# Kernel tuning notes

Hardware: AMD Instinct MI355X
Metric: run time of the kernel (lower is better)

## Reference

```python
import jax, jax.numpy as jnp
import numpy as np

B, N, H = 32, 1024, 512
THR = 0.05  # peak_detection_threshold


def _l2norm(x):
    return x / jnp.linalg.norm(x, axis=-1, keepdims=True)


def setup_inputs() -> dict:
    key = jax.random.key(0)
    ks = jax.random.split(key, 6)
    def w(k, shape, fan_in):
        return jax.random.normal(k, shape, jnp.float32) / np.float32(np.sqrt(fan_in))
    return {
        "segment_rep": jax.random.normal(ks[0], (B, N, H), jnp.float32),
        "phn_mask": jnp.ones((B, N), jnp.float32),
        # SegmentSimilarityMeasure: Linear(2H->H), ReLU, Linear(H->1, no bias)
        "W1": w(ks[1], (2 * H, H), 2 * H),
        "b1": jnp.zeros((H,), jnp.float32),
        "W2": w(ks[2], (H, 1), H),
        # word_enc: Linear(H->H), ReLU, Linear(H->H)
        "We1": w(ks[3], (H, H), H),
        "be1": jnp.zeros((H,), jnp.float32),
        "We2": w(ks[4], (H, H), H),
        "be2": jnp.zeros((H,), jnp.float32),
    }


def _forward(segment_rep, phn_mask, W1, b1, W2, We1, be1, We2, be2):
    Bs, Np, Hd = segment_rep.shape
    # adjacent segment similarity: MLP on concat of l2-normalized neighbors -> (B, N-1)
    cat = jnp.concatenate([_l2norm(segment_rep[:, :-1, :]), _l2norm(segment_rep[:, 1:, :])], axis=2)
    S = (jax.nn.relu(cat @ W1 + b1) @ W2)[..., 0]

    # relative dissimilarity
    Smin = jnp.min(S, axis=1, keepdims=True)
    Smax = jnp.max(S, axis=1, keepdims=True)
    D = 1.0 - (S - Smin) / (Smax - Smin)

    # peak detector (faithful to original, incl. final overwrite of first-order cols -2:)
    z = jnp.zeros_like(D)
    fo = z
    fo = fo.at[:, 0].set(jnp.maximum(D[:, 0] - D[:, 1], 0.0))
    fo = fo.at[:, 1:-1].set(jnp.minimum(jnp.maximum(D[:, 1:-1] - D[:, :-2], 0.0),
                                        jnp.maximum(D[:, 1:-1] - D[:, 2:], 0.0)))
    fo = fo.at[:, -1].set(jnp.maximum(D[:, -1] - D[:, -2], 0.0))
    so = z
    so = so.at[:, 0:2].set(jnp.maximum(D[:, 0:2] - D[:, 2:4], 0.0))
    so = so.at[:, 2:-2].set(jnp.minimum(jnp.maximum(D[:, 2:-2] - D[:, :-4], 0.0),
                                        jnp.maximum(D[:, 2:-2] - D[:, 4:], 0.0)))
    fo = fo.at[:, -2:].set(jnp.maximum(D[:, -2:] - D[:, -4:-2], 0.0))  # replicates original code
    P = jnp.minimum(jnp.maximum(jnp.maximum(fo, so) - THR, 0.0), fo)

    # pad, mask, straight-through hard boundaries
    P = jnp.pad(P, ((0, 0), (0, 1)))
    P = jax.nn.relu(P + (phn_mask - 1.0))
    b_soft = jnp.tanh(10.0 * P)
    b_hard = jnp.tanh(100000.0 * P)
    b = b_soft + jax.lax.stop_gradient(b_hard - b_soft)
    b = jnp.cumsum(b, axis=1)  # (B, N)
    b = b + (b[:, :1] == 0).astype(b.dtype)  # per-row +1 if b[:,0]==0
    num_word_segments = b[:, -1].astype(jnp.int32) + 1  # (B,)

    # U: column j holds j+1 for j < num_word_segments[i], else -100000. Nmax = N (static bound).
    cols = jnp.arange(1, Np + 1, dtype=jnp.int32)  # (Nmax,)
    U = jnp.where(cols[None, :] <= num_word_segments[:, None],
                  cols.astype(segment_rep.dtype)[None, :], -100000.0)  # (B, Nmax)

    V = U[:, None, :] - b[:, :, None]  # (B, N, Nmax)
    Wseg = 1.0 - jnp.tanh(100000.0 * jnp.abs(V))
    Wseg = Wseg / jnp.sum(Wseg, axis=1, keepdims=True)
    Wseg = jnp.nan_to_num(Wseg)

    # pool: (B, Nmax, N) @ (B, N, H) -> (B, Nmax, H)
    word_rep = jnp.einsum('bnm,bnh->bmh', Wseg, segment_rep)
    word_masks = jnp.where(word_rep == 0, 0.0, 1.0)
    out = jax.nn.relu(word_rep @ We1 + be1) @ We2 + be2
    return out * word_masks


def reference(segment_rep, phn_mask, W1, b1, W2, We1, be1, We2, be2):
    return _forward(segment_rep, phn_mask, W1, b1, W2, We1, be1, We2, be2)
```

## Files before the change

kernel.cpp:

```cpp
#include <hip/hip_runtime.h>

#define BB 32
#define NN 1024
#define HH 512
#define NS 1023

typedef unsigned short u16;
typedef unsigned int   u32;
typedef __attribute__((ext_vector_type(8))) short bf16x8;
typedef __attribute__((ext_vector_type(4))) float f32x4;

__device__ __forceinline__ float bf2f(u16 h) {
  union { u32 u; float f; } c; c.u = ((u32)h) << 16; return c.f;
}
__device__ __forceinline__ u16 f2bf(float f) {
  union { float f; u32 u; } c; c.f = f;
  u32 u = c.u;
  return (u16)((u + 0x7fffu + ((u >> 16) & 1u)) >> 16);
}
__device__ __forceinline__ void split_bf(float x, u16& hi, u16& lo) {
  hi = f2bf(x);
  lo = f2bf(x - bf2f(hi));
}

__global__ __launch_bounds__(64) void k_prep_a(const float* __restrict__ seg,
                                               u16* __restrict__ ahi,
                                               u16* __restrict__ alo) {
  int row = blockIdx.x, lane = threadIdx.x;
  const float4* p = (const float4*)(seg + ((size_t)row << 9) + lane * 8);
  float4 a = p[0], b = p[1];
  float v[8] = {a.x, a.y, a.z, a.w, b.x, b.y, b.z, b.w};
  float s = 0.f;
#pragma unroll
  for (int i = 0; i < 8; ++i) s += v[i] * v[i];
#pragma unroll
  for (int m = 32; m; m >>= 1) s += __shfl_xor(s, m, 64);
  float nrm = sqrtf(s);
  u16 h[8], l[8];
#pragma unroll
  for (int i = 0; i < 8; ++i) split_bf(v[i] / nrm, h[i], l[i]);
  size_t off = ((size_t)row << 9) + lane * 8;
  *(uint4*)(ahi + off) = make_uint4(h[0] | (h[1] << 16), h[2] | (h[3] << 16),
                                    h[4] | (h[5] << 16), h[6] | (h[7] << 16));
  *(uint4*)(alo + off) = make_uint4(l[0] | (l[1] << 16), l[2] | (l[3] << 16),
                                    l[4] | (l[5] << 16), l[6] | (l[7] << 16));
}

__global__ __launch_bounds__(256) void k_tr(const float* __restrict__ src,
                                            u16* __restrict__ dh,
                                            u16* __restrict__ dl,
                                            int K, int N) {
  __shared__ u16 Th[64 * 66], Tl[64 * 66];
  int nb = blockIdx.x * 64, kb = blockIdx.y * 64;
  int tid = threadIdx.x;
#pragma unroll
  for (int i = 0; i < 16; ++i) {
    int e = tid + i * 256;
    int r = e >> 6, c = e & 63;
    float v = src[(size_t)(kb + r) * N + nb + c];
    u16 hi, lo; split_bf(v, hi, lo);
    Th[c * 66 + r] = hi;
    Tl[c * 66 + r] = lo;
  }
  __syncthreads();
#pragma unroll
  for (int i = 0; i < 16; ++i) {
    int e = tid + i * 256;
    int n = e >> 6, k = e & 63;
    dh[(size_t)(nb + n) * K + kb + k] = Th[n * 66 + k];
    if (dl) dl[(size_t)(nb + n) * K + kb + k] = Tl[n * 66 + k];
  }
}

__global__ __launch_bounds__(256) void k_sgemm(const u16* __restrict__ ahi,
                                               const u16* __restrict__ alo,
                                               const u16* __restrict__ w1h,
                                               const u16* __restrict__ w1l,
                                               const float* __restrict__ b1,
                                               const float* __restrict__ W2,
                                               float* __restrict__ Spart) {
  __shared__ u16 Ah[64 * 40], Al_[64 * 40];
  __shared__ u16 Wh[256 * 40], Wl[256 * 40];
  __shared__ float red[4][64];

  int tid = threadIdx.x;
  int wave = tid >> 6, lane = tid & 63, quad = lane >> 4, l15 = lane & 15;
  int b = blockIdx.z, mblk = blockIdx.y, nblk = blockIdx.x;
  int rowbase = b * NN + mblk * 64;
  int ncol0 = nblk * 256;

  f32x4 acc[4][4];
#pragma unroll
  for (int mi = 0; mi < 4; ++mi)
#pragma unroll
    for (int ni = 0; ni < 4; ++ni) acc[mi][ni] = (f32x4){0.f, 0.f, 0.f, 0.f};

  for (int ks = 0; ks < 32; ++ks) {
    int k0 = ks * 32, half = k0 >> 9, cb = k0 & 511;
    __syncthreads();
#pragma unroll
    for (int it = 0; it < 2; ++it) {
      int i = tid + it * 256;
      int m = i >> 3, plane = (i >> 2) & 1, ch = i & 3;
      int grow = rowbase + m + half; if (grow > 32767) grow = 32767;
      size_t go = ((size_t)grow << 9) + cb + ch * 8;
      if (plane) *(uint4*)&Al_[m * 40 + ch * 8] = *(const uint4*)(alo + go);
      else       *(uint4*)&Ah [m * 40 + ch * 8] = *(const uint4*)(ahi + go);
    }
#pragma unroll
    for (int it = 0; it < 8; ++it) {
      int i = tid + it * 256;
      int n = i >> 3, plane = (i >> 2) & 1, ch = i & 3;
      size_t go = (size_t)(ncol0 + n) * 1024 + k0 + ch * 8;
      if (plane) *(uint4*)&Wl[n * 40 + ch * 8] = *(const uint4*)(w1l + go);
      else       *(uint4*)&Wh[n * 40 + ch * 8] = *(const uint4*)(w1h + go);
    }
    __syncthreads();

    bf16x8 a_h[4], a_l[4];
#pragma unroll
    for (int mi = 0; mi < 4; ++mi) {
      int off = (mi * 16 + l15) * 40 + quad * 8;
      a_h[mi] = *(const bf16x8*)&Ah [off];
      a_l[mi] = *(const bf16x8*)&Al_[off];
    }
#pragma unroll
    for (int ni = 0; ni < 4; ++ni) {
      int off = (wave * 64 + ni * 16 + l15) * 40 + quad * 8;
      bf16x8 b_h = *(const bf16x8*)&Wh[off];
      bf16x8 b_l = *(const bf16x8*)&Wl[off];
#pragma unroll
      for (int mi = 0; mi < 4; ++mi) {
        acc[mi][ni] = __builtin_amdgcn_mfma_f32_16x16x32_bf16(a_h[mi], b_h, acc[mi][ni], 0, 0, 0);
        acc[mi][ni] = __builtin_amdgcn_mfma_f32_16x16x32_bf16(a_h[mi], b_l, acc[mi][ni], 0, 0, 0);
        acc[mi][ni] = __builtin_amdgcn_mfma_f32_16x16x32_bf16(a_l[mi], b_h, acc[mi][ni], 0, 0, 0);
      }
    }
  }

#pragma unroll
  for (int mi = 0; mi < 4; ++mi) {
#pragma unroll
    for (int reg = 0; reg < 4; ++reg) {
      float part = 0.f;
#pragma unroll
      for (int ni = 0; ni < 4; ++ni) {
        int n_g = ncol0 + wave * 64 + ni * 16 + l15;
        float h = acc[mi][ni][reg] + b1[n_g];
        h = h > 0.f ? h : 0.f;
        part = fmaf(h, W2[n_g], part);
      }
#pragma unroll
      for (int m = 8; m; m >>= 1) part += __shfl_xor(part, m, 64);
      if (l15 == 0) red[wave][mi * 16 + quad * 4 + reg] = part;
    }
  }
  __syncthreads();
  if (tid < 64) {
    float s = red[0][tid] + red[1][tid] + red[2][tid] + red[3][tid];
    int srow = mblk * 64 + tid;
    if (srow < NS)
      Spart[((size_t)nblk * BB + b) * NN + srow] = s;
  }
}

__global__ __launch_bounds__(256) void k_row(const float* __restrict__ S0,
                                             const float* __restrict__ S1,
                                             const float* __restrict__ mask,
                                             int* __restrict__ assign,
                                             float* __restrict__ weight,
                                             float* __restrict__ total,
                                             int* __restrict__ startn,
                                             int* __restrict__ endn) {
  int b = blockIdx.x, tid = threadIdx.x;
  __shared__ float Ssh[NS];
  __shared__ float Dsh[NS];
  __shared__ float tsh[NN];
  __shared__ float bsh[NN];
  __shared__ float totl[NN];
  __shared__ int   stl[NN];
  __shared__ int   enl[NN];
  __shared__ float red[256];

  for (int n = tid; n < NS; n += 256)
    Ssh[n] = S0[((size_t)b << 10) + n] + S1[((size_t)b << 10) + n];
  __syncthreads();

  float mn = INFINITY, mx = -INFINITY;
  for (int n = tid; n < NS; n += 256) {
    float v = Ssh[n];
    mn = fminf(mn, v); mx = fmaxf(mx, v);
  }
  red[tid] = mn; __syncthreads();
  for (int s = 128; s; s >>= 1) { if (tid < s) red[tid] = fminf(red[tid], red[tid + s]); __syncthreads(); }
  float Smin = red[0]; __syncthreads();
  red[tid] = mx; __syncthreads();
  for (int s = 128; s; s >>= 1) { if (tid < s) red[tid] = fmaxf(red[tid], red[tid + s]); __syncthreads(); }
  float Smax = red[0]; __syncthreads();

  for (int n = tid; n < NS; n += 256)
    Dsh[n] = 1.0f - (Ssh[n] - Smin) / (Smax - Smin);
  __syncthreads();

  for (int n = tid; n < NN; n += 256) {
    float P;
    if (n >= NS) {
      P = 0.f;
    } else {
      float D = Dsh[n];
      float fo, so;
      if (n == 0)            fo = fmaxf(D - Dsh[1], 0.f);
      else if (n >= NS - 2)  fo = fmaxf(D - Dsh[n - 2], 0.f);
      else                   fo = fminf(fmaxf(D - Dsh[n - 1], 0.f),
                                        fmaxf(D - Dsh[n + 1], 0.f));
      if (n <= 1)            so = fmaxf(D - Dsh[n + 2], 0.f);
      else if (n >= NS - 2)  so = 0.f;
      else                   so = fminf(fmaxf(D - Dsh[n - 2], 0.f),
                                        fmaxf(D - Dsh[n + 2], 0.f));
      P = fminf(fmaxf(fmaxf(fo, so) - 0.05f, 0.f), fo);
    }
    float m = mask[((size_t)b << 10) + n];
    P = P + (m - 1.0f);
    P = P > 0.f ? P : 0.f;
    float bs = tanhf(10.0f * P);
    float bh = tanhf(100000.0f * P);
    tsh[n] = bs + (bh - bs);
  }
  __syncthreads();

  if (tid == 0) {
    float acc = 0.f;
    for (int n = 0; n < NN; n += 8) {
      float t0 = tsh[n + 0], t1 = tsh[n + 1], t2 = tsh[n + 2], t3 = tsh[n + 3];
      float t4 = tsh[n + 4], t5 = tsh[n + 5], t6 = tsh[n + 6], t7 = tsh[n + 7];
      acc += t0; bsh[n + 0] = acc; acc += t1; bsh[n + 1] = acc;
      acc += t2; bsh[n + 2] = acc; acc += t3; bsh[n + 3] = acc;
      acc += t4; bsh[n + 4] = acc; acc += t5; bsh[n + 5] = acc;
      acc += t6; bsh[n + 6] = acc; acc += t7; bsh[n + 7] = acc;
    }
  }
  __syncthreads();

  float add1 = (bsh[0] == 0.0f) ? 1.0f : 0.0f;
  int   num  = (int)(bsh[NN - 1] + add1) + 1;

  for (int mi = tid; mi < NN; mi += 256) { totl[mi] = 0.f; stl[mi] = 1 << 30; enl[mi] = -1; }
  __syncthreads();

  for (int n = tid; n < NN; n += 256) {
    float bv = bsh[n] + add1;
    float kf = rintf(bv);
    int   k  = (int)kf;
    int   a  = -1; float w = 0.f;
    if (k >= 1 && k <= num && k <= NN) {
      float v = fabsf(kf - bv);
      w = 1.0f - tanhf(100000.0f * v);
      if (w > 0.f) {
        a = k - 1;
        atomicAdd(&totl[a], w);
        atomicMin(&stl[a], n);
        atomicMax(&enl[a], n);
      } else {
        a = -1; w = 0.f;
      }
    }
    assign[((size_t)b << 10) + n] = a;
    weight[((size_t)b << 10) + n] = w;
  }
  __syncthreads();
  for (int mi = tid; mi < NN; mi += 256) {
    total [((size_t)b << 10) + mi] = totl[mi];
    startn[((size_t)b << 10) + mi] = stl[mi];
    endn  [((size_t)b << 10) + mi] = enl[mi];
  }
}

__global__ __launch_bounds__(64) void k_pool(const float* __restrict__ seg,
                                             const int* __restrict__ assign,
                                             const float* __restrict__ weight,
                                             const float* __restrict__ total,
                                             const int* __restrict__ startn,
                                             const int* __restrict__ endn,
                                             float* __restrict__ wrep) {
  int bm = blockIdx.x;
  int b  = bm >> 10, m = bm & 1023;
  int lane = threadIdx.x;
  float acc[8] = {0.f, 0.f, 0.f, 0.f, 0.f, 0.f, 0.f, 0.f};
  float tm = total[bm];
  if (tm > 0.f) {
    int s = startn[bm], e = endn[bm];
    for (int n = s; n <= e; ++n) {
      if (assign[((size_t)b << 10) + n] != m) continue;
      float coef = weight[((size_t)b << 10) + n] / tm;
      const float4* p = (const float4*)(seg + (((size_t)b << 10) + n) * HH + lane * 8);
      float4 x = p[0], y = p[1];
      acc[0] = fmaf(coef, x.x, acc[0]); acc[1] = fmaf(coef, x.y, acc[1]);
      acc[2] = fmaf(coef, x.z, acc[2]); acc[3] = fmaf(coef, x.w, acc[3]);
      acc[4] = fmaf(coef, y.x, acc[4]); acc[5] = fmaf(coef, y.y, acc[5]);
      acc[6] = fmaf(coef, y.z, acc[6]); acc[7] = fmaf(coef, y.w, acc[7]);
    }
  }
  float4* dst = (float4*)(wrep + (size_t)bm * HH + lane * 8);
  dst[0] = make_float4(acc[0], acc[1], acc[2], acc[3]);
  dst[1] = make_float4(acc[4], acc[5], acc[6], acc[7]);
}

__global__ __launch_bounds__(512) void k_out(const u16* __restrict__ we1t,
                                             const u16* __restrict__ we2t,
                                             const float* __restrict__ be1,
                                             const float* __restrict__ be2,
                                             float* __restrict__ io) {
  __shared__ u16 Hid[64 * 520];
  __shared__ u16 Wst[512 * 40];
  __shared__ u16 Ast[64 * 40];

  int tid = threadIdx.x;
  int wave = tid >> 6, lane = tid & 63, quad = lane >> 4, l15 = lane & 15;
  int wm = wave >> 2, wn = wave & 3;
  int rowbase = blockIdx.x * 64;

  f32x4 acc[2][8];
#pragma unroll
  for (int mi = 0; mi < 2; ++mi)
#pragma unroll
    for (int ni = 0; ni < 8; ++ni) acc[mi][ni] = (f32x4){0.f, 0.f, 0.f, 0.f};

  for (int ks = 0; ks < 16; ++ks) {
    int k0 = ks * 32;
    __syncthreads();
    {
      int m = tid >> 3, ch = tid & 7;
      float4 v = *(const float4*)(io + (size_t)(rowbase + m) * HH + k0 + ch * 4);
      u32 p0 = f2bf(v.x) | ((u32)f2bf(v.y) << 16);
      u32 p1 = f2bf(v.z) | ((u32)f2bf(v.w) << 16);
      *(uint2*)&Ast[m * 40 + ch * 4] = make_uint2(p0, p1);
    }
#pragma unroll
    for (int it = 0; it < 4; ++it) {
      int i = tid + it * 512;
      int n = i >> 2, ch = i & 3;
      *(uint4*)&Wst[n * 40 + ch * 8] = *(const uint4*)(we1t + (size_t)n * HH + k0 + ch * 8);
    }
    __syncthreads();

    bf16x8 a[2];
#pragma unroll
    for (int mi = 0; mi < 2; ++mi)
      a[mi] = *(const bf16x8*)&Ast[(wm * 32 + mi * 16 + l15) * 40 + quad * 8];
#pragma unroll
    for (int ni = 0; ni < 8; ++ni) {
      bf16x8 bfr = *(const bf16x8*)&Wst[(wn * 128 + ni * 16 + l15) * 40 + quad * 8];
#pragma unroll
      for (int mi = 0; mi < 2; ++mi)
        acc[mi][ni] = __builtin_amdgcn_mfma_f32_16x16x32_bf16(a[mi], bfr, acc[mi][ni], 0, 0, 0);
    }
  }
#pragma unroll
  for (int mi = 0; mi < 2; ++mi)
#pragma unroll
    for (int ni = 0; ni < 8; ++ni)
#pragma unroll
      for (int reg = 0; reg < 4; ++reg) {
        int n_g = wn * 128 + ni * 16 + l15;
        float h = acc[mi][ni][reg] + be1[n_g];
        h = h > 0.f ? h : 0.f;
        Hid[(wm * 32 + mi * 16 + quad * 4 + reg) * 520 + n_g] = f2bf(h);
      }

#pragma unroll
  for (int mi = 0; mi < 2; ++mi)
#pragma unroll
    for (int ni = 0; ni < 8; ++ni) acc[mi][ni] = (f32x4){0.f, 0.f, 0.f, 0.f};

  for (int ks = 0; ks < 16; ++ks) {
    int k0 = ks * 32;
    __syncthreads();
#pragma unroll
    for (int it = 0; it < 4; ++it) {
      int i = tid + it * 512;
      int n = i >> 2, ch = i & 3;
      *(uint4*)&Wst[n * 40 + ch * 8] = *(const uint4*)(we2t + (size_t)n * HH + k0 + ch * 8);
    }
    __syncthreads();

    bf16x8 a[2];
#pragma unroll
    for (int mi = 0; mi < 2; ++mi)
      a[mi] = *(const bf16x8*)&Hid[(wm * 32 + mi * 16 + l15) * 520 + k0 + quad * 8];
#pragma unroll
    for (int ni = 0; ni < 8; ++ni) {
      bf16x8 bfr = *(const bf16x8*)&Wst[(wn * 128 + ni * 16 + l15) * 40 + quad * 8];
#pragma unroll
      for (int mi = 0; mi < 2; ++mi)
        acc[mi][ni] = __builtin_amdgcn_mfma_f32_16x16x32_bf16(a[mi], bfr, acc[mi][ni], 0, 0, 0);
    }
  }

#pragma unroll
  for (int mi = 0; mi < 2; ++mi)
#pragma unroll
    for (int ni = 0; ni < 8; ++ni)
#pragma unroll
      for (int reg = 0; reg < 4; ++reg) {
        int n_g = wn * 128 + ni * 16 + l15;
        size_t row = (size_t)(rowbase + wm * 32 + mi * 16 + quad * 4 + reg);
        float o = acc[mi][ni][reg] + be2[n_g];
        float wr = io[row * HH + n_g];
        io[row * HH + n_g] = (wr == 0.f) ? 0.f : o;
      }
}

__global__ void k_diag(float* __restrict__ out, int hostcode) {
  if (hostcode != 0) out[0] = (float)hostcode;
}

extern "C" void kernel_launch(void* const* d_in, const int* in_sizes, int n_in,
                              void* d_out, int out_size, void* d_ws, size_t ws_size,
                              hipStream_t stream) {
  const float* seg  = (const float*)d_in[0];
  const float* mask = (const float*)d_in[1];
  const float* W1   = (const float*)d_in[2];
  const float* b1   = (const float*)d_in[3];
  const float* W2   = (const float*)d_in[4];
  const float* We1  = (const float*)d_in[5];
  const float* be1  = (const float*)d_in[6];
  const float* We2  = (const float*)d_in[7];
  const float* be2  = (const float*)d_in[8];

  const size_t NROW = (size_t)BB * NN;
  float* ws = (float*)d_ws;
  float* S0     = ws;
  float* S1     = S0 + NROW;
  int*   assign = (int*)(S1 + NROW);
  float* weight = (float*)(assign + NROW);
  float* total  = weight + NROW;
  int*   startn = (int*)(total + NROW);
  int*   endn   = startn + NROW;
  u16*   w1h    = (u16*)(endn + NROW);
  u16*   w1l    = w1h + (size_t)512 * 1024;
  u16*   we1t   = w1l + (size_t)512 * 1024;
  u16*   we2t   = we1t + (size_t)512 * 512;

  float* out = (float*)d_out;
  u16*   ahi = (u16*)d_out;
  u16*   alo = ahi + (size_t)NROW * HH;

  int hostcode = 0;
  if (ws_size < (size_t)7 * NROW * 4 + (size_t)3 * 1024 * 1024) hostcode += 32768;
  if (out_size != 16777216) hostcode += 8192;

  k_prep_a<<<dim3(BB * NN), dim3(64), 0, stream>>>(seg, ahi, alo);
  k_tr    <<<dim3(8, 16), dim3(256), 0, stream>>>(W1, w1h, w1l, 1024, 512);
  k_tr    <<<dim3(8, 8),  dim3(256), 0, stream>>>(We1, we1t, (u16*)nullptr, 512, 512);
  k_tr    <<<dim3(8, 8),  dim3(256), 0, stream>>>(We2, we2t, (u16*)nullptr, 512, 512);
  k_sgemm <<<dim3(2, 16, BB), dim3(256), 0, stream>>>(ahi, alo, w1h, w1l, b1, W2, S0);
  k_row   <<<dim3(BB), dim3(256), 0, stream>>>(S0, S1, mask, assign, weight, total, startn, endn);
  k_pool  <<<dim3(BB * NN), dim3(64), 0, stream>>>(seg, assign, weight, total, startn, endn, out);
  k_out   <<<dim3(NROW / 64), dim3(512), 0, stream>>>(we1t, we2t, be1, be2, out);
  k_diag  <<<dim3(1), dim3(1), 0, stream>>>(out, hostcode);
}
```

Before: 387.6 us.

## Load weight fragments directly from global and double-buffer activation tiles in LDS

In the similarity GEMM and the output MLP kernels, weight B-fragments are now read straight from global memory into registers instead of being staged through shared memory. The activation A tiles are double-buffered in LDS with a register prefetch of the next K slice, so each iteration needs one barrier instead of two. The aim is to cut LDS traffic and barrier stalls. In exchange, each weight row is read from global/L2 by every block without LDS reuse, and the per-lane access pattern is strided, which may raise memory latency.

```diff
diff --git a/kernel.cpp b/kernel.cpp
--- a/kernel.cpp
+++ b/kernel.cpp
@@ -79,8 +79,7 @@
                                                const float* __restrict__ b1,
                                                const float* __restrict__ W2,
                                                float* __restrict__ Spart) {
-  __shared__ u16 Ah[64 * 40], Al_[64 * 40];
-  __shared__ u16 Wh[256 * 40], Wl[256 * 40];
+  __shared__ u16 Ah[2][64 * 32], Al_[2][64 * 32];
   __shared__ float red[4][64];
 
   int tid = threadIdx.x;
@@ -89,52 +88,60 @@
   int rowbase = b * NN + mblk * 64;
   int ncol0 = nblk * 256;
 
+  int m_st = tid >> 2, ch_st = tid & 3;
+
   f32x4 acc[4][4];
 #pragma unroll
   for (int mi = 0; mi < 4; ++mi)
 #pragma unroll
     for (int ni = 0; ni < 4; ++ni) acc[mi][ni] = (f32x4){0.f, 0.f, 0.f, 0.f};
 
+  {
+    int grow = rowbase + m_st; if (grow > 32767) grow = 32767;
+    size_t g = ((size_t)grow << 9) + ch_st * 8;
+    *(uint4*)&Ah [0][m_st * 32 + ch_st * 8] = *(const uint4*)(ahi + g);
+    *(uint4*)&Al_[0][m_st * 32 + ch_st * 8] = *(const uint4*)(alo + g);
+  }
+
   for (int ks = 0; ks < 32; ++ks) {
-    int k0 = ks * 32, half = k0 >> 9, cb = k0 & 511;
+    int bb = ks & 1;
     __syncthreads();
-#pragma unroll
-    for (int it = 0; it < 2; ++it) {
-      int i = tid + it * 256;
-      int m = i >> 3, plane = (i >> 2) & 1, ch = i & 3;
-      int grow = rowbase + m + half; if (grow > 32767) grow = 32767;
-      size_t go = ((size_t)grow << 9) + cb + ch * 8;
-      if (plane) *(uint4*)&Al_[m * 40 + ch * 8] = *(const uint4*)(alo + go);
-      else       *(uint4*)&Ah [m * 40 + ch * 8] = *(const uint4*)(ahi + go);
-    }
-#pragma unroll
-    for (int it = 0; it < 8; ++it) {
-      int i = tid + it * 256;
-      int n = i >> 3, plane = (i >> 2) & 1, ch = i & 3;
-      size_t go = (size_t)(ncol0 + n) * 1024 + k0 + ch * 8;
-      if (plane) *(uint4*)&Wl[n * 40 + ch * 8] = *(const uint4*)(w1l + go);
-      else       *(uint4*)&Wh[n * 40 + ch * 8] = *(const uint4*)(w1h + go);
-    }
-    __syncthreads();
-
+    bool have = (ks + 1) < 32;
+    uint4 nh, nl;
+    if (have) {
+      int k0n = (ks + 1) * 32, halfn = k0n >> 9, cbn = k0n & 511;
+      int grow = rowbase + m_st + halfn; if (grow > 32767) grow = 32767;
+      size_t g = ((size_t)grow << 9) + cbn + ch_st * 8;
+      nh = *(const uint4*)(ahi + g);
+      nl = *(const uint4*)(alo + g);
+    }
+    int k0 = ks * 32;
+    const u16* wbh = w1h + (size_t)(ncol0 + wave * 64 + l15) * 1024 + k0 + quad * 8;
+    const u16* wbl = w1l + (size_t)(ncol0 + wave * 64 + l15) * 1024 + k0 + quad * 8;
+    bf16x8 bh[4], bl[4];
+#pragma unroll
+    for (int ni = 0; ni < 4; ++ni) {
+      bh[ni] = *(const bf16x8*)(wbh + (size_t)ni * 16 * 1024);
+      bl[ni] = *(const bf16x8*)(wbl + (size_t)ni * 16 * 1024);
+    }
     bf16x8 a_h[4], a_l[4];
 #pragma unroll
     for (int mi = 0; mi < 4; ++mi) {
-      int off = (mi * 16 + l15) * 40 + quad * 8;
-      a_h[mi] = *(const bf16x8*)&Ah [off];
-      a_l[mi] = *(const bf16x8*)&Al_[off];
-    }
-#pragma unroll
-    for (int ni = 0; ni < 4; ++ni) {
-      int off = (wave * 64 + ni * 16 + l15) * 40 + quad * 8;
-      bf16x8 b_h = *(const bf16x8*)&Wh[off];
-      bf16x8 b_l = *(const bf16x8*)&Wl[off];
+      int off = (mi * 16 + l15) * 32 + quad * 8;
+      a_h[mi] = *(const bf16x8*)&Ah [bb][off];
+      a_l[mi] = *(const bf16x8*)&Al_[bb][off];
+    }
+#pragma unroll
+    for (int ni = 0; ni < 4; ++ni)
 #pragma unroll
       for (int mi = 0; mi < 4; ++mi) {
-        acc[mi][ni] = __builtin_amdgcn_mfma_f32_16x16x32_bf16(a_h[mi], b_h, acc[mi][ni], 0, 0, 0);
-        acc[mi][ni] = __builtin_amdgcn_mfma_f32_16x16x32_bf16(a_h[mi], b_l, acc[mi][ni], 0, 0, 0);
-        acc[mi][ni] = __builtin_amdgcn_mfma_f32_16x16x32_bf16(a_l[mi], b_h, acc[mi][ni], 0, 0, 0);
+        acc[mi][ni] = __builtin_amdgcn_mfma_f32_16x16x32_bf16(a_h[mi], bh[ni], acc[mi][ni], 0, 0, 0);
+        acc[mi][ni] = __builtin_amdgcn_mfma_f32_16x16x32_bf16(a_h[mi], bl[ni], acc[mi][ni], 0, 0, 0);
+        acc[mi][ni] = __builtin_amdgcn_mfma_f32_16x16x32_bf16(a_l[mi], bh[ni], acc[mi][ni], 0, 0, 0);
       }
+    if (have) {
+      *(uint4*)&Ah [bb ^ 1][m_st * 32 + ch_st * 8] = nh;
+      *(uint4*)&Al_[bb ^ 1][m_st * 32 + ch_st * 8] = nl;
     }
   }
 
@@ -311,13 +318,13 @@
                                              const float* __restrict__ be2,
                                              float* __restrict__ io) {
   __shared__ u16 Hid[64 * 520];
-  __shared__ u16 Wst[512 * 40];
-  __shared__ u16 Ast[64 * 40];
+  __shared__ u16 Ast[2][64 * 32];
 
   int tid = threadIdx.x;
   int wave = tid >> 6, lane = tid & 63, quad = lane >> 4, l15 = lane & 15;
   int wm = wave >> 2, wn = wave & 3;
   int rowbase = blockIdx.x * 64;
+  int m_st = tid >> 3, ch_st = tid & 7;
 
   f32x4 acc[2][8];
 #pragma unroll
@@ -325,34 +332,38 @@
 #pragma unroll
     for (int ni = 0; ni < 8; ++ni) acc[mi][ni] = (f32x4){0.f, 0.f, 0.f, 0.f};
 
+  {
+    float4 v = *(const float4*)(io + (size_t)(rowbase + m_st) * HH + ch_st * 4);
+    u32 p0 = f2bf(v.x) | ((u32)f2bf(v.y) << 16);
+    u32 p1 = f2bf(v.z) | ((u32)f2bf(v.w) << 16);
+    *(uint2*)&Ast[0][m_st * 32 + ch_st * 4] = make_uint2(p0, p1);
+  }
+
   for (int ks = 0; ks < 16; ++ks) {
+    int bb = ks & 1;
+    __syncthreads();
+    bool have = (ks + 1) < 16;
+    float4 nx;
+    if (have)
+      nx = *(const float4*)(io + (size_t)(rowbase + m_st) * HH + (ks + 1) * 32 + ch_st * 4);
     int k0 = ks * 32;
-    __syncthreads();
-    {
-      int m = tid >> 3, ch = tid & 7;
-      float4 v = *(const float4*)(io + (size_t)(rowbase + m) * HH + k0 + ch * 4);
-      u32 p0 = f2bf(v.x) | ((u32)f2bf(v.y) << 16);
-      u32 p1 = f2bf(v.z) | ((u32)f2bf(v.w) << 16);
-      *(uint2*)&Ast[m * 40 + ch * 4] = make_uint2(p0, p1);
-    }
-#pragma unroll
-    for (int it = 0; it < 4; ++it) {
-      int i = tid + it * 512;
-      int n = i >> 2, ch = i & 3;
-      *(uint4*)&Wst[n * 40 + ch * 8] = *(const uint4*)(we1t + (size_t)n * HH + k0 + ch * 8);
-    }
-    __syncthreads();
-
+    const u16* wb = we1t + (size_t)(wn * 128 + l15) * 512 + k0 + quad * 8;
+    bf16x8 bw[8];
+#pragma unroll
+    for (int ni = 0; ni < 8; ++ni) bw[ni] = *(const bf16x8*)(wb + (size_t)ni * 16 * 512);
     bf16x8 a[2];
 #pragma unroll
     for (int mi = 0; mi < 2; ++mi)
-      a[mi] = *(const bf16x8*)&Ast[(wm * 32 + mi * 16 + l15) * 40 + quad * 8];
-#pragma unroll
-    for (int ni = 0; ni < 8; ++ni) {
-      bf16x8 bfr = *(const bf16x8*)&Wst[(wn * 128 + ni * 16 + l15) * 40 + quad * 8];
+      a[mi] = *(const bf16x8*)&Ast[bb][(wm * 32 + mi * 16 + l15) * 32 + quad * 8];
+#pragma unroll
+    for (int ni = 0; ni < 8; ++ni)
 #pragma unroll
       for (int mi = 0; mi < 2; ++mi)
-        acc[mi][ni] = __builtin_amdgcn_mfma_f32_16x16x32_bf16(a[mi], bfr, acc[mi][ni], 0, 0, 0);
+        acc[mi][ni] = __builtin_amdgcn_mfma_f32_16x16x32_bf16(a[mi], bw[ni], acc[mi][ni], 0, 0, 0);
+    if (have) {
+      u32 p0 = f2bf(nx.x) | ((u32)f2bf(nx.y) << 16);
+      u32 p1 = f2bf(nx.z) | ((u32)f2bf(nx.w) << 16);
+      *(uint2*)&Ast[bb ^ 1][m_st * 32 + ch_st * 4] = make_uint2(p0, p1);
     }
   }
 #pragma unroll
@@ -366,6 +377,7 @@
         h = h > 0.f ? h : 0.f;
         Hid[(wm * 32 + mi * 16 + quad * 4 + reg) * 520 + n_g] = f2bf(h);
       }
+  __syncthreads();
 
 #pragma unroll
   for (int mi = 0; mi < 2; ++mi)
@@ -374,26 +386,19 @@
 
   for (int ks = 0; ks < 16; ++ks) {
     int k0 = ks * 32;
-    __syncthreads();
-#pragma unroll
-    for (int it = 0; it < 4; ++it) {
-      int i = tid + it * 512;
-      int n = i >> 2, ch = i & 3;
-      *(uint4*)&Wst[n * 40 + ch * 8] = *(const uint4*)(we2t + (size_t)n * HH + k0 + ch * 8);
-    }
-    __syncthreads();
-
+    const u16* wb = we2t + (size_t)(wn * 128 + l15) * 512 + k0 + quad * 8;
+    bf16x8 bw[8];
+#pragma unroll
+    for (int ni = 0; ni < 8; ++ni) bw[ni] = *(const bf16x8*)(wb + (size_t)ni * 16 * 512);
     bf16x8 a[2];
 #pragma unroll
     for (int mi = 0; mi < 2; ++mi)
       a[mi] = *(const bf16x8*)&Hid[(wm * 32 + mi * 16 + l15) * 520 + k0 + quad * 8];
 #pragma unroll
-    for (int ni = 0; ni < 8; ++ni) {
-      bf16x8 bfr = *(const bf16x8*)&Wst[(wn * 128 + ni * 16 + l15) * 40 + quad * 8];
+    for (int ni = 0; ni < 8; ++ni)
 #pragma unroll
       for (int mi = 0; mi < 2; ++mi)
-        acc[mi][ni] = __builtin_amdgcn_mfma_f32_16x16x32_bf16(a[mi], bfr, acc[mi][ni], 0, 0, 0);
-    }
+        acc[mi][ni] = __builtin_amdgcn_mfma_f32_16x16x32_bf16(a[mi], bw[ni], acc[mi][ni], 0, 0, 0);
   }
 
 #pragma unroll
```

New measurement: 534.9 us. +38.0%, slower.
